# Performance work log

Hardware: AMD Instinct MI355X
Metric: run time of the kernel (lower is better)

Reference implementation:

```python
import jax, jax.numpy as jnp
import numpy as np

NBIT = 8
NSPLIT = 255.0  # 2**NBIT - 1


def _quantized_matmul(x, w_clean, eps):
    # Faithful port of quantization(): bit-slice x into NBIT binary planes, run a
    # noisy linear per plane with weight w + randn*|w|*0.1, and sum. The 8
    # sequential fc() calls are fused into one einsum over the bit axis.
    # x: (..., in); w_clean: (out, in); eps: (NBIT, out, in) standard normal.
    mn = jnp.min(x)
    mx = jnp.max(x)
    q = ((x - mn) / (mx - mn) * NSPLIT).astype(jnp.uint8).astype(jnp.int32)  # truncating cast as in torch
    quant_base = 2 ** jnp.arange(NBIT, dtype=jnp.int32)
    binary = ((q[..., None] & quant_base) != 0).astype(x.dtype)              # (..., in, NBIT)
    scaled = binary * (2.0 ** jnp.arange(NBIT)).astype(x.dtype)              # plane i scaled by 2**i
    w_noisy = w_clean[None] + eps * jnp.abs(w_clean)[None] * 0.1             # (NBIT, out, in)
    z = jnp.einsum('...ib,boi->...o', scaled, w_noisy)
    return z, mn, mx, w_noisy[-1]  # fc.weight after loop == last noisy weight


def _forward(node_embedding, edge_embedding, nbr_mask, cond1, cond2, eps1, eps2, bn_gamma, bn_beta):
    B, At, Nbr, Fe = edge_embedding.shape
    Fn = node_embedding.shape[-1]
    c1 = jnp.concatenate(
        [jnp.broadcast_to(node_embedding[:, :, None, :], (B, At, Nbr, Fn)), edge_embedding],
        axis=3)                                                              # (B, At, Nbr, Fn+Fe)
    # quantization + re_quantization through fc (re-quant uses last noisy fc.weight)
    z1, mn1, mx1, w_last = _quantized_matmul(c1, cond1[0], eps1)
    bias1 = jnp.sum(mn1 * w_last, axis=1)                                    # (H1,)
    h = jax.nn.relu(z1 / NSPLIT * (mx1 - mn1) + bias1)                       # (B, At, Nbr, H1)
    # quantization + re_quantization through fc_2 (re-quant uses conductance[1][-1])
    z2, mn2, mx2, _ = _quantized_matmul(h, cond2[0], eps2)
    bias2 = jnp.sum(mn2 * cond2[-1], axis=1)                                 # (2*Fn,)
    c2 = z2 / NSPLIT * (mx2 - mn2) + bias2                                   # (B, At, Nbr, 2*Fn)
    nbr_gate, nbr_extract = jnp.split(c2, 2, axis=3)
    nbr_sumed = jax.nn.sigmoid(nbr_gate) * jnp.tanh(nbr_extract) * nbr_mask[..., None]
    nbr_sumed = jnp.sum(nbr_sumed, axis=2)                                   # (B, At, Fn)
    # BatchNorm1d in training mode: batch statistics over flattened (B*At)
    flat = nbr_sumed.reshape(-1, Fn)
    mean = jnp.mean(flat, axis=0)
    var = jnp.var(flat, axis=0)  # biased variance, as torch BN uses for normalization
    bn = ((flat - mean) / jnp.sqrt(var + 1e-5) * bn_gamma + bn_beta).reshape(B, At, Fn)
    return jax.nn.relu(node_embedding + bn)


def setup_inputs() -> dict:
    key = jax.random.key(0)
    ks = jax.random.split(key, 7)
    B, At, Nbr, Fn, Fe = 16, 96, 12, 64, 64
    H1, H2 = 4 * (Fn + Fe), 2 * Fn
    return {
        'node_embedding': jax.random.normal(ks[0], (B, At, Fn), jnp.float32),
        'edge_embedding': jax.random.normal(ks[1], (B, At, Nbr, Fe), jnp.float32),
        'nbr_mask': (jax.random.uniform(ks[2], (B, At, Nbr)) > 0.5).astype(jnp.float32),
        'cond1': jax.random.normal(ks[3], (2, H1, Fn + Fe), jnp.float32) * 0.05,
        'cond2': jax.random.normal(ks[4], (2, H2, H1), jnp.float32) * 0.05,
        'eps1': jax.random.normal(ks[5], (NBIT, H1, Fn + Fe), jnp.float32),
        'eps2': jax.random.normal(ks[6], (NBIT, H2, H1), jnp.float32),
        'bn_gamma': jnp.ones((Fn,), jnp.float32),
        'bn_beta': jnp.zeros((Fn,), jnp.float32),
    }


def reference(node_embedding, edge_embedding, nbr_mask, cond1, cond2, eps1, eps2, bn_gamma, bn_beta):
    return _forward(node_embedding, edge_embedding, nbr_mask, cond1, cond2, eps1, eps2, bn_gamma, bn_beta)
```

## Files before the change

kernel.cpp:

```cpp
#include <hip/hip_runtime.h>
#include <stdint.h>

#define B_    16
#define AT_   96
#define NBR_  12
#define FN_   64
#define FE_   64
#define M1    (B_*AT_*NBR_)
#define R_    (B_*AT_)
#define K1Q   128
#define N1    512
#define K2Q   512
#define N2    128
#define SPLIT2 4

typedef _Float16 f16x8 __attribute__((ext_vector_type(8)));
typedef float    f32x4 __attribute__((ext_vector_type(4)));
typedef __attribute__((address_space(1))) const void gconst_void;
typedef __attribute__((address_space(3))) void lds_void;

#define OFF_SCAL  0u
#define OFF_B1R   256u
#define OFF_B2R   (OFF_B1R + 2048u)
#define OFF_Q1    4096u
#define OFF_W1E   (OFF_Q1  + (size_t)M1*K1Q)
#define OFF_W2E   (OFF_W1E + (size_t)N1*K1Q*8*2)
#define OFF_Q2    (OFF_W2E + (size_t)N2*K2Q*8*2)
#define OFF_H     (OFF_Q2  + (size_t)M1*K2Q)
#define OFF_ZP    OFF_H
#define OFF_NS    (OFF_H   + (size_t)M1*N1*4)

__device__ __forceinline__ unsigned int enc_f(float f) {
    unsigned int u = __float_as_uint(f);
    return (u & 0x80000000u) ? ~u : (u | 0x80000000u);
}
__device__ __forceinline__ float dec_f(unsigned int u) {
    return __uint_as_float((u & 0x80000000u) ? (u & 0x7FFFFFFFu) : ~u);
}

__global__ void k_init(unsigned int* scal, float* b1raw, float* b2raw) {
    int t = threadIdx.x;
    if (t == 0) { scal[0] = 0xFFFFFFFFu; scal[1] = 0u; scal[2] = 0xFFFFFFFFu; scal[3] = 0u; }
    if (t < N1) b1raw[t] = 0.f;
    if (t < N2) b2raw[t] = 0.f;
}

__global__ __launch_bounds__(256) void k_minmax_c1(const float* __restrict__ node,
                                                   const float* __restrict__ edge,
                                                   unsigned int* __restrict__ scal) {
    const int nn = B_*AT_*FN_;
    const int ntot = nn + M1*FE_;
    float mn = 3.0e38f, mx = -3.0e38f;
    for (int idx = blockIdx.x*blockDim.x + threadIdx.x; idx < ntot; idx += gridDim.x*blockDim.x) {
        float x = (idx < nn) ? node[idx] : edge[idx - nn];
        mn = fminf(mn, x); mx = fmaxf(mx, x);
    }
    __shared__ float smn[256], smx[256];
    smn[threadIdx.x] = mn; smx[threadIdx.x] = mx; __syncthreads();
    for (int s = 128; s > 0; s >>= 1) {
        if (threadIdx.x < s) {
            smn[threadIdx.x] = fminf(smn[threadIdx.x], smn[threadIdx.x+s]);
            smx[threadIdx.x] = fmaxf(smx[threadIdx.x], smx[threadIdx.x+s]);
        }
        __syncthreads();
    }
    if (threadIdx.x == 0) { atomicMin(&scal[0], enc_f(smn[0])); atomicMax(&scal[1], enc_f(smx[0])); }
}

template<int KQ, int N, int SBASE, bool USE_SECOND>
__global__ __launch_bounds__(256) void k_prep_w16(const float* __restrict__ w_clean,
                                                  const float* __restrict__ eps,
                                                  const unsigned int* __restrict__ scal,
                                                  float* __restrict__ braw,
                                                  _Float16* __restrict__ We) {
    int idx = blockIdx.x*blockDim.x + threadIdx.x;
    if (idx >= N*KQ) return;
    int o = idx / KQ;
    float mn = dec_f(scal[SBASE]), mx = dec_f(scal[SBASE+1]);
    float s = (mx - mn) * (1.0f/255.0f);
    float w = w_clean[idx];
    float aw = fabsf(w) * 0.1f;
    union { _Float16 h[8]; uint4 u; } pk;
    float p = s;
    float v7 = 0.f;
    #pragma unroll
    for (int b = 0; b < 8; b++) {
        float e = eps[(size_t)b*N*KQ + idx];
        float v = w + e*aw;
        if (b == 7) v7 = v;
        pk.h[b] = (_Float16)(v * p);
        p *= 2.0f;
    }
    *(uint4*)&We[(size_t)idx*8] = pk.u;
    float bv = USE_SECOND ? w_clean[(size_t)N*KQ + idx] : v7;
    #pragma unroll
    for (int off = 32; off > 0; off >>= 1) bv += __shfl_down(bv, off);
    if ((threadIdx.x & 63) == 0) atomicAdd(&braw[o], bv);
}

__global__ __launch_bounds__(256) void k_quant_c1(const float* __restrict__ node,
                                                  const float* __restrict__ edge,
                                                  const unsigned int* __restrict__ scal,
                                                  unsigned int* __restrict__ qt) {
    __shared__ unsigned int T[128*33];
    const int mblk = blockIdx.x, t = threadIdx.x;
    const float mn = dec_f(scal[0]), rng = dec_f(scal[1]) - mn;
    #pragma unroll
    for (int r = 0; r < 16; ++r) {
        int p = r*256 + t;
        int row = p >> 5, c4 = p & 31, j = c4*4;
        int m = mblk*128 + row;
        float4 x = (j < 64) ? *(const float4*)&node[(m/NBR_)*FN_ + j]
                            : *(const float4*)&edge[(size_t)m*FE_ + (j-64)];
        unsigned int b0 = (unsigned char)(int)((x.x - mn) / rng * 255.0f);
        unsigned int b1 = (unsigned char)(int)((x.y - mn) / rng * 255.0f);
        unsigned int b2 = (unsigned char)(int)((x.z - mn) / rng * 255.0f);
        unsigned int b3 = (unsigned char)(int)((x.w - mn) / rng * 255.0f);
        T[row*33 + c4] = b0 | (b1 << 8) | (b2 << 16) | (b3 << 24);
    }
    __syncthreads();
    #pragma unroll
    for (int r = 0; r < 16; ++r) {
        int o = r*256 + t;
        qt[(size_t)mblk*4096 + o] = T[(t>>1)*33 + r*2 + (t&1)];
    }
}

__global__ __launch_bounds__(256) void k_quant_h(const float* __restrict__ h,
                                                 const unsigned int* __restrict__ scal,
                                                 unsigned int* __restrict__ qt) {
    __shared__ unsigned int T[128*33];
    const int mblk = blockIdx.x, jc = blockIdx.y, t = threadIdx.x;
    const float mn = dec_f(scal[2]), rng = dec_f(scal[3]) - mn;
    #pragma unroll
    for (int r = 0; r < 16; ++r) {
        int p = r*256 + t;
        int row = p >> 5, c4 = p & 31;
        float4 x = *(const float4*)&h[(size_t)(mblk*128 + row)*512 + jc*128 + c4*4];
        unsigned int b0 = (unsigned char)(int)((x.x - mn) / rng * 255.0f);
        unsigned int b1 = (unsigned char)(int)((x.y - mn) / rng * 255.0f);
        unsigned int b2 = (unsigned char)(int)((x.z - mn) / rng * 255.0f);
        unsigned int b3 = (unsigned char)(int)((x.w - mn) / rng * 255.0f);
        T[row*33 + c4] = b0 | (b1 << 8) | (b2 << 16) | (b3 << 24);
    }
    __syncthreads();
    #pragma unroll
    for (int r = 0; r < 16; ++r) {
        int o = r*256 + t;
        qt[(size_t)mblk*16384 + (size_t)jc*4096 + o] = T[(t>>1)*33 + r*2 + (t&1)];
    }
}

__device__ __forceinline__ f16x8 expand_byte(unsigned int byte) {
    unsigned int r2 = byte | (byte << 15);
    union { unsigned int u[4]; f16x8 h; } t;
    t.u[0] = ( r2       & 0x00010001u) * 0x3C00u;
    t.u[1] = ((r2 >> 2) & 0x00010001u) * 0x3C00u;
    t.u[2] = ((r2 >> 4) & 0x00010001u) * 0x3C00u;
    t.u[3] = ((r2 >> 6) & 0x00010001u) * 0x3C00u;
    return t.h;
}

template<int KQ, int N, int SPLITK, bool EPI1>
__global__ __launch_bounds__(256, 4) void kg(const unsigned char* __restrict__ q,
                                             const _Float16* __restrict__ W,
                                             const float* __restrict__ braw,
                                             void* __restrict__ outv,
                                             unsigned int* __restrict__ scal) {
    constexpr int KP  = KQ * 8;
    constexpr int KPS = KP / SPLITK;
    constexpr int NIT = KPS / 128;
    __shared__ _Float16 Bs[16384];
    __shared__ __align__(16) unsigned char As[16384];

    const int tid  = threadIdx.x;
    const int lane = tid & 63;
    const int w    = tid >> 6;
    const int wm   = (w & 1) * 64;
    const int kg   = w >> 1;
    const int l15  = lane & 15;
    const int lq   = lane >> 4;
    const int sh8  = lq * 8;
    const int m0   = blockIdx.x * 128;
    const int o0   = blockIdx.y * 64;
    const int kbase = blockIdx.z * KPS;

    f32x4 acc[4][4] = {};

    unsigned int bo[4];
    #pragma unroll
    for (int iss = 0; iss < 4; ++iss) {
        int s = iss*256 + tid, skg = s >> 9, sg = s & 511, n = sg >> 3;
        int csrc = (sg & 7) ^ (n & 7);
        bo[iss] = (unsigned int)((o0 + n)*KP + kbase + skg*512 + csrc*8);
    }
    const int bdl = (tid & ~63) * 8;

    const unsigned char* aq = q + (size_t)blockIdx.x*((size_t)KQ*128) + (size_t)blockIdx.z*16384;
    #pragma unroll
    for (int r = 0; r < 4; ++r)
        __builtin_amdgcn_global_load_lds((gconst_void*)(aq + r*4096 + tid*16),
            (lds_void*)(As + r*4096 + (tid & ~63)*16), 16, 0, 0);

    auto stageB = [&](int IT, int BUF) {
        #pragma unroll
        for (int iss = 0; iss < 4; ++iss)
            __builtin_amdgcn_global_load_lds((gconst_void*)(W + bo[iss] + IT*64),
                (lds_void*)(Bs + BUF*8192 + iss*2048 + bdl), 16, 0, 0);
    };

    auto compute = [&](int cur, int it) {
        const _Float16* Bc = Bs + cur*8192 + kg*4096;
        const unsigned char* Ac = As + kg*8192 + it*1024;
        uint2 qd[4];
        #pragma unroll
        for (int mf = 0; mf < 4; ++mf)
            qd[mf] = *(const uint2*)&Ac[(wm + mf*16 + l15)*8];
        #pragma unroll
        for (int kf = 0; kf < 2; ++kf) {
            f16x8 bf[4];
            #pragma unroll
            for (int nf = 0; nf < 4; ++nf) {
                const int nl = nf*16 + l15;
                const int ch = kf*4 + lq;
                bf[nf] = *(const f16x8*)&Bc[nl*64 + ((ch ^ (nl & 7)) << 3)];
            }
            __builtin_amdgcn_s_setprio(1);
            #pragma unroll
            for (int mf = 0; mf < 4; ++mf) {
                unsigned int byte = ((kf ? qd[mf].y : qd[mf].x) >> sh8) & 0xFFu;
                f16x8 a = expand_byte(byte);
                #pragma unroll
                for (int nf = 0; nf < 4; ++nf)
                    acc[mf][nf] = __builtin_amdgcn_mfma_f32_16x16x32_f16(a, bf[nf], acc[mf][nf], 0, 0, 0);
            }
            __builtin_amdgcn_s_setprio(0);
        }
    };

    stageB(0, 0);
    #pragma unroll 1
    for (int it = 0; it < NIT-1; ++it) {
        const int cur = it & 1;
        stageB(it+1, cur ^ 1);
        asm volatile("s_waitcnt vmcnt(4)" ::: "memory");
        asm volatile("s_barrier" ::: "memory");
        compute(cur, it);
        asm volatile("s_waitcnt lgkmcnt(0)" ::: "memory");
        asm volatile("s_barrier" ::: "memory");
    }
    asm volatile("s_waitcnt vmcnt(0)" ::: "memory");
    asm volatile("s_barrier" ::: "memory");
    compute((NIT-1) & 1, NIT-1);

    float* red = (float*)Bs;
    #pragma unroll
    for (int nf = 0; nf < 4; ++nf) {
        __syncthreads();
        if (kg == 1) {
            #pragma unroll
            for (int mf = 0; mf < 4; ++mf)
                *(f32x4*)&red[(w & 1)*1024 + mf*256 + lane*4] = acc[mf][nf];
        }
        __syncthreads();
        if (kg == 0) {
            #pragma unroll
            for (int mf = 0; mf < 4; ++mf)
                acc[mf][nf] += *(const f32x4*)&red[(w & 1)*1024 + mf*256 + lane*4];
        }
    }

    if (EPI1) {
        float tmn = 3.0e38f, tmx = -3.0e38f;
        if (kg == 0) {
            float* out = (float*)outv;
            const float mn1 = dec_f(scal[0]);
            float bv[4];
            #pragma unroll
            for (int nf = 0; nf < 4; ++nf) bv[nf] = mn1 * braw[o0 + nf*16 + l15];
            #pragma unroll
            for (int mf = 0; mf < 4; ++mf) {
                const int mr = m0 + wm + mf*16 + lq*4;
                #pragma unroll
                for (int nf = 0; nf < 4; ++nf) {
                    const int oc = o0 + nf*16 + l15;
                    #pragma unroll
                    for (int r = 0; r < 4; ++r) {
                        float v = acc[mf][nf][r] + bv[nf];
                        v = fmaxf(v, 0.0f);
                        tmn = fminf(tmn, v); tmx = fmaxf(tmx, v);
                        out[(size_t)(mr + r)*N + oc] = v;
                    }
                }
            }
        }
        __syncthreads();
        red[tid] = tmn; red[256 + tid] = tmx;
        __syncthreads();
        for (int s = 128; s > 0; s >>= 1) {
            if (tid < s) {
                red[tid]       = fminf(red[tid],       red[tid + s]);
                red[256 + tid] = fmaxf(red[256 + tid], red[256 + tid + s]);
            }
            __syncthreads();
        }
        if (tid == 0) { atomicMin(&scal[2], enc_f(red[0])); atomicMax(&scal[3], enc_f(red[256])); }
    } else {
        if (kg == 0) {
            _Float16* op = (_Float16*)outv + (size_t)blockIdx.z * ((size_t)M1 * N);
            #pragma unroll
            for (int mf = 0; mf < 4; ++mf) {
                const int mr = m0 + wm + mf*16 + lq*4;
                #pragma unroll
                for (int nf = 0; nf < 4; ++nf) {
                    const int oc = o0 + nf*16 + l15;
                    #pragma unroll
                    for (int r = 0; r < 4; ++r)
                        op[(size_t)(mr + r)*N + oc] = (_Float16)acc[mf][nf][r];
                }
            }
        }
    }
}

__global__ __launch_bounds__(256) void k_nbr(const _Float16* __restrict__ zp,
                                             const float* __restrict__ b2raw,
                                             const unsigned int* __restrict__ scal,
                                             const float* __restrict__ mask,
                                             float* __restrict__ ns) {
    const size_t SP = (size_t)M1 * N2;
    int tid = threadIdx.x;
    int r = blockIdx.x*4 + (tid >> 6);
    int f = tid & 63;
    const float mn2 = dec_f(scal[2]);
    float bg = mn2 * b2raw[f], be = mn2 * b2raw[64 + f];
    float s = 0.f;
    #pragma unroll
    for (int n = 0; n < NBR_; n++) {
        int m = r*NBR_ + n;
        size_t base = (size_t)m * N2;
        float g = bg, e = be;
        #pragma unroll
        for (int z = 0; z < SPLIT2; z++) {
            g += (float)zp[z*SP + base + f];
            e += (float)zp[z*SP + base + 64 + f];
        }
        float sig = 1.0f / (1.0f + expf(-g));
        s += sig * tanhf(e) * mask[m];
    }
    ns[r*64 + f] = s;
}

__global__ __launch_bounds__(256) void k_bn(const float* __restrict__ ns,
                                            const float* __restrict__ node,
                                            const float* __restrict__ gamma,
                                            const float* __restrict__ beta,
                                            float* __restrict__ out) {
    int f = blockIdx.x;
    int tid = threadIdx.x;
    float x[6];
    float s = 0.f, ss = 0.f;
    #pragma unroll
    for (int k = 0; k < 6; k++) {
        int r = tid + k*256;
        x[k] = ns[r*64 + f];
        s += x[k]; ss += x[k]*x[k];
    }
    __shared__ float rs[256], rss[256];
    rs[tid] = s; rss[tid] = ss; __syncthreads();
    for (int st = 128; st > 0; st >>= 1) {
        if (tid < st) { rs[tid] += rs[tid+st]; rss[tid] += rss[tid+st]; }
        __syncthreads();
    }
    float mean = rs[0] / 1536.0f;
    float var  = rss[0] / 1536.0f - mean*mean;
    float denom = sqrtf(var + 1e-5f);
    float g = gamma[f], bt = beta[f];
    #pragma unroll
    for (int k = 0; k < 6; k++) {
        int r = tid + k*256;
        float v = node[r*64 + f] + ((x[k] - mean) / denom * g + bt);
        out[r*64 + f] = fmaxf(v, 0.f);
    }
}

extern "C" void kernel_launch(void* const* d_in, const int* in_sizes, int n_in,
                              void* d_out, int out_size, void* d_ws, size_t ws_size,
                              hipStream_t stream) {
    const float* node  = (const float*)d_in[0];
    const float* edge  = (const float*)d_in[1];
    const float* mask  = (const float*)d_in[2];
    const float* cond1 = (const float*)d_in[3];
    const float* cond2 = (const float*)d_in[4];
    const float* eps1  = (const float*)d_in[5];
    const float* eps2  = (const float*)d_in[6];
    const float* gamma = (const float*)d_in[7];
    const float* beta  = (const float*)d_in[8];
    float* out = (float*)d_out;
    char* ws = (char*)d_ws;

    unsigned int*  scal = (unsigned int*)(ws + OFF_SCAL);
    float* b1raw = (float*)(ws + OFF_B1R);
    float* b2raw = (float*)(ws + OFF_B2R);
    unsigned char* q1 = (unsigned char*)(ws + OFF_Q1);
    _Float16* W1e = (_Float16*)(ws + OFF_W1E);
    _Float16* W2e = (_Float16*)(ws + OFF_W2E);
    unsigned char* q2 = (unsigned char*)(ws + OFF_Q2);
    float*    h  = (float*)(ws + OFF_H);
    _Float16* zp = (_Float16*)(ws + OFF_ZP);
    float*    ns = (float*)(ws + OFF_NS);

    k_init<<<1, 1024, 0, stream>>>(scal, b1raw, b2raw);
    k_minmax_c1<<<512, 256, 0, stream>>>(node, edge, scal);
    k_prep_w16<K1Q, N1, 0, false><<<(N1*K1Q + 255)/256, 256, 0, stream>>>(cond1, eps1, scal, b1raw, W1e);
    k_quant_c1<<<M1/128, 256, 0, stream>>>(node, edge, scal, (unsigned int*)q1);
    kg<K1Q, N1, 1, true><<<dim3(M1/128, N1/64, 1), 256, 0, stream>>>(q1, W1e, b1raw, h, scal);
    k_prep_w16<K2Q, N2, 2, true><<<(N2*K2Q + 255)/256, 256, 0, stream>>>(cond2, eps2, scal, b2raw, W2e);
    k_quant_h<<<dim3(M1/128, 4), 256, 0, stream>>>(h, scal, (unsigned int*)q2);
    kg<K2Q, N2, SPLIT2, false><<<dim3(M1/128, N2/64, SPLIT2), 256, 0, stream>>>(q2, W2e, b2raw, zp, scal);
    k_nbr<<<R_/4, 256, 0, stream>>>(zp, b2raw, scal, mask, ns);
    k_bn<<<64, 256, 0, stream>>>(ns, node, gamma, beta, out);
}
```

Baseline: 218.5 us.

## Replace LDS-staged block GEMM with single-wave direct-global-load GEMM

The bit-plane GEMM moves from 256-thread blocks, which stage A and B tiles through LDS with double buffering, intra-block split-K and an LDS reduction, to single-wave 64-thread blocks. Each wave now loads its A bytes and B fragments straight from global memory into registers and computes a 64x64 tile over the full K slice. The LDS barriers, the cross-wave reduction and the tree min/max are dropped, and the min/max uses a wave shuffle reduction instead. The cost is less data reuse through LDS, so more global and L2 traffic from uncoalesced per-lane fragment loads. It also gives up the explicit prefetch pipelining and launches more, smaller blocks.

Result: slower. 280.0 us (+28.2%).

```diff
diff --git a/kernel.cpp b/kernel.cpp
--- a/kernel.cpp
+++ b/kernel.cpp
@@ -16,8 +16,6 @@
 
 typedef _Float16 f16x8 __attribute__((ext_vector_type(8)));
 typedef float    f32x4 __attribute__((ext_vector_type(4)));
-typedef __attribute__((address_space(1))) const void gconst_void;
-typedef __attribute__((address_space(3))) void lds_void;
 
 #define OFF_SCAL  0u
 #define OFF_B1R   256u
@@ -162,70 +160,44 @@
 }
 
 template<int KQ, int N, int SPLITK, bool EPI1>
-__global__ __launch_bounds__(256, 4) void kg(const unsigned char* __restrict__ q,
+__global__ __launch_bounds__(64, 4) void kgw(const unsigned char* __restrict__ q,
                                              const _Float16* __restrict__ W,
                                              const float* __restrict__ braw,
                                              void* __restrict__ outv,
                                              unsigned int* __restrict__ scal) {
     constexpr int KP  = KQ * 8;
     constexpr int KPS = KP / SPLITK;
-    constexpr int NIT = KPS / 128;
-    __shared__ _Float16 Bs[16384];
-    __shared__ __align__(16) unsigned char As[16384];
-
-    const int tid  = threadIdx.x;
-    const int lane = tid & 63;
-    const int w    = tid >> 6;
-    const int wm   = (w & 1) * 64;
-    const int kg   = w >> 1;
-    const int l15  = lane & 15;
-    const int lq   = lane >> 4;
-    const int sh8  = lq * 8;
-    const int m0   = blockIdx.x * 128;
-    const int o0   = blockIdx.y * 64;
-    const int kbase = blockIdx.z * KPS;
+    constexpr int NJG = KPS / 64;
+
+    const int lane = threadIdx.x;
+    const int l15 = lane & 15;
+    const int lq  = lane >> 4;
+    const int sh8 = lq * 8;
+    const int mt  = blockIdx.x;
+    const int o0  = blockIdx.y * 64;
+    const int z   = blockIdx.z;
 
     f32x4 acc[4][4] = {};
 
-    unsigned int bo[4];
-    #pragma unroll
-    for (int iss = 0; iss < 4; ++iss) {
-        int s = iss*256 + tid, skg = s >> 9, sg = s & 511, n = sg >> 3;
-        int csrc = (sg & 7) ^ (n & 7);
-        bo[iss] = (unsigned int)((o0 + n)*KP + kbase + skg*512 + csrc*8);
-    }
-    const int bdl = (tid & ~63) * 8;
-
-    const unsigned char* aq = q + (size_t)blockIdx.x*((size_t)KQ*128) + (size_t)blockIdx.z*16384;
-    #pragma unroll
-    for (int r = 0; r < 4; ++r)
-        __builtin_amdgcn_global_load_lds((gconst_void*)(aq + r*4096 + tid*16),
-            (lds_void*)(As + r*4096 + (tid & ~63)*16), 16, 0, 0);
-
-    auto stageB = [&](int IT, int BUF) {
-        #pragma unroll
-        for (int iss = 0; iss < 4; ++iss)
-            __builtin_amdgcn_global_load_lds((gconst_void*)(W + bo[iss] + IT*64),
-                (lds_void*)(Bs + BUF*8192 + iss*2048 + bdl), 16, 0, 0);
-    };
-
-    auto compute = [&](int cur, int it) {
-        const _Float16* Bc = Bs + cur*8192 + kg*4096;
-        const unsigned char* Ac = As + kg*8192 + it*1024;
+    const unsigned char* aq = q + (size_t)(mt >> 1)*((size_t)KQ*128)
+                                + (size_t)z*16384 + ((mt & 1)*64 + l15)*8;
+    const _Float16* wn[4];
+    #pragma unroll
+    for (int nf = 0; nf < 4; ++nf)
+        wn[nf] = W + (size_t)(o0 + nf*16 + l15)*KP + (size_t)z*KPS + lq*8;
+
+    #pragma unroll 2
+    for (int jg = 0; jg < NJG; ++jg) {
         uint2 qd[4];
         #pragma unroll
         for (int mf = 0; mf < 4; ++mf)
-            qd[mf] = *(const uint2*)&Ac[(wm + mf*16 + l15)*8];
+            qd[mf] = *(const uint2*)(aq + jg*1024 + mf*128);
         #pragma unroll
         for (int kf = 0; kf < 2; ++kf) {
             f16x8 bf[4];
             #pragma unroll
-            for (int nf = 0; nf < 4; ++nf) {
-                const int nl = nf*16 + l15;
-                const int ch = kf*4 + lq;
-                bf[nf] = *(const f16x8*)&Bc[nl*64 + ((ch ^ (nl & 7)) << 3)];
-            }
-            __builtin_amdgcn_s_setprio(1);
+            for (int nf = 0; nf < 4; ++nf)
+                bf[nf] = *(const f16x8*)(wn[nf] + jg*64 + kf*32);
             #pragma unroll
             for (int mf = 0; mf < 4; ++mf) {
                 unsigned int byte = ((kf ? qd[mf].y : qd[mf].x) >> sh8) & 0xFFu;
@@ -234,90 +206,48 @@
                 for (int nf = 0; nf < 4; ++nf)
                     acc[mf][nf] = __builtin_amdgcn_mfma_f32_16x16x32_f16(a, bf[nf], acc[mf][nf], 0, 0, 0);
             }
-            __builtin_amdgcn_s_setprio(0);
-        }
-    };
-
-    stageB(0, 0);
-    #pragma unroll 1
-    for (int it = 0; it < NIT-1; ++it) {
-        const int cur = it & 1;
-        stageB(it+1, cur ^ 1);
-        asm volatile("s_waitcnt vmcnt(4)" ::: "memory");
-        asm volatile("s_barrier" ::: "memory");
-        compute(cur, it);
-        asm volatile("s_waitcnt lgkmcnt(0)" ::: "memory");
-        asm volatile("s_barrier" ::: "memory");
-    }
-    asm volatile("s_waitcnt vmcnt(0)" ::: "memory");
-    asm volatile("s_barrier" ::: "memory");
-    compute((NIT-1) & 1, NIT-1);
-
-    float* red = (float*)Bs;
-    #pragma unroll
-    for (int nf = 0; nf < 4; ++nf) {
-        __syncthreads();
-        if (kg == 1) {
+        }
+    }
+
+    if (EPI1) {
+        float* out = (float*)outv;
+        const float mn1 = dec_f(scal[0]);
+        float bv[4];
+        #pragma unroll
+        for (int nf = 0; nf < 4; ++nf) bv[nf] = mn1 * braw[o0 + nf*16 + l15];
+        float tmn = 3.0e38f, tmx = -3.0e38f;
+        #pragma unroll
+        for (int mf = 0; mf < 4; ++mf) {
+            const int mr = mt*64 + mf*16 + lq*4;
             #pragma unroll
-            for (int mf = 0; mf < 4; ++mf)
-                *(f32x4*)&red[(w & 1)*1024 + mf*256 + lane*4] = acc[mf][nf];
-        }
-        __syncthreads();
-        if (kg == 0) {
-            #pragma unroll
-            for (int mf = 0; mf < 4; ++mf)
-                acc[mf][nf] += *(const f32x4*)&red[(w & 1)*1024 + mf*256 + lane*4];
-        }
-    }
-
-    if (EPI1) {
-        float tmn = 3.0e38f, tmx = -3.0e38f;
-        if (kg == 0) {
-            float* out = (float*)outv;
-            const float mn1 = dec_f(scal[0]);
-            float bv[4];
-            #pragma unroll
-            for (int nf = 0; nf < 4; ++nf) bv[nf] = mn1 * braw[o0 + nf*16 + l15];
-            #pragma unroll
-            for (int mf = 0; mf < 4; ++mf) {
-                const int mr = m0 + wm + mf*16 + lq*4;
+            for (int nf = 0; nf < 4; ++nf) {
+                const int oc = o0 + nf*16 + l15;
                 #pragma unroll
-                for (int nf = 0; nf < 4; ++nf) {
-                    const int oc = o0 + nf*16 + l15;
-                    #pragma unroll
-                    for (int r = 0; r < 4; ++r) {
-                        float v = acc[mf][nf][r] + bv[nf];
-                        v = fmaxf(v, 0.0f);
-                        tmn = fminf(tmn, v); tmx = fmaxf(tmx, v);
-                        out[(size_t)(mr + r)*N + oc] = v;
-                    }
+                for (int r = 0; r < 4; ++r) {
+                    float v = acc[mf][nf][r] + bv[nf];
+                    v = fmaxf(v, 0.0f);
+                    tmn = fminf(tmn, v); tmx = fmaxf(tmx, v);
+                    out[(size_t)(mr + r)*N + oc] = v;
                 }
             }
         }
-        __syncthreads();
-        red[tid] = tmn; red[256 + tid] = tmx;
-        __syncthreads();
-        for (int s = 128; s > 0; s >>= 1) {
-            if (tid < s) {
-                red[tid]       = fminf(red[tid],       red[tid + s]);
-                red[256 + tid] = fmaxf(red[256 + tid], red[256 + tid + s]);
-            }
-            __syncthreads();
-        }
-        if (tid == 0) { atomicMin(&scal[2], enc_f(red[0])); atomicMax(&scal[3], enc_f(red[256])); }
+        #pragma unroll
+        for (int off = 32; off > 0; off >>= 1) {
+            tmn = fminf(tmn, __shfl_xor(tmn, off));
+            tmx = fmaxf(tmx, __shfl_xor(tmx, off));
+        }
+        if (lane == 0) { atomicMin(&scal[2], enc_f(tmn)); atomicMax(&scal[3], enc_f(tmx)); }
     } else {
-        if (kg == 0) {
-            _Float16* op = (_Float16*)outv + (size_t)blockIdx.z * ((size_t)M1 * N);
+        _Float16* op = (_Float16*)outv + (size_t)z * ((size_t)M1 * N);
+        #pragma unroll
+        for (int mf = 0; mf < 4; ++mf) {
+            const int mr = mt*64 + mf*16 + lq*4;
             #pragma unroll
-            for (int mf = 0; mf < 4; ++mf) {
-                const int mr = m0 + wm + mf*16 + lq*4;
+            for (int nf = 0; nf < 4; ++nf) {
+                const int oc = o0 + nf*16 + l15;
                 #pragma unroll
-                for (int nf = 0; nf < 4; ++nf) {
-                    const int oc = o0 + nf*16 + l15;
-                    #pragma unroll
-                    for (int r = 0; r < 4; ++r)
-                        op[(size_t)(mr + r)*N + oc] = (_Float16)acc[mf][nf][r];
-                }
+                for (int r = 0; r < 4; ++r)
+                    op[(size_t)(mr + r)*N + oc] = (_Float16)acc[mf][nf][r];
             }
         }
     }
@@ -414,10 +344,10 @@
     k_minmax_c1<<<512, 256, 0, stream>>>(node, edge, scal);
     k_prep_w16<K1Q, N1, 0, false><<<(N1*K1Q + 255)/256, 256, 0, stream>>>(cond1, eps1, scal, b1raw, W1e);
     k_quant_c1<<<M1/128, 256, 0, stream>>>(node, edge, scal, (unsigned int*)q1);
-    kg<K1Q, N1, 1, true><<<dim3(M1/128, N1/64, 1), 256, 0, stream>>>(q1, W1e, b1raw, h, scal);
+    kgw<K1Q, N1, 1, true><<<dim3(M1/64, N1/64, 1), 64, 0, stream>>>(q1, W1e, b1raw, h, scal);
     k_prep_w16<K2Q, N2, 2, true><<<(N2*K2Q + 255)/256, 256, 0, stream>>>(cond2, eps2, scal, b2raw, W2e);
     k_quant_h<<<dim3(M1/128, 4), 256, 0, stream>>>(h, scal, (unsigned int*)q2);
-    kg<K2Q, N2, SPLIT2, false><<<dim3(M1/128, N2/64, SPLIT2), 256, 0, stream>>>(q2, W2e, b2raw, zp, scal);
+    kgw<K2Q, N2, SPLIT2, false><<<dim3(M1/64, N2/64, SPLIT2), 64, 0, stream>>>(q2, W2e, b2raw, zp, scal);
     k_nbr<<<R_/4, 256, 0, stream>>>(zp, b2raw, scal, mask, ns);
     k_bn<<<64, 256, 0, stream>>>(ns, node, gamma, beta, out);
 }
```

## Split GEMM warps over N, triple-buffer B tiles, add XCD-aware block swizzle

Applied to the files above, without the earlier changes.

The GEMM kernel no longer splits K across warp pairs, which required an LDS reduction at the end. The four warps now split the N dimension, each computing a 64x32 tile. B staging moves to a 3-deep ring of 64-wide K chunks, so compute overlaps with two outstanding prefetches. The 3D grid becomes a 1D grid whose block index is remapped to group neighbouring tiles on the same XCD for L2 reuse. In exchange there are twice as many K iterations, each with more barriers, and every wave now does per-wave epilogue stores.

After: 212.5 us. 2.7% less time.

```diff
diff --git a/kernel.cpp b/kernel.cpp
--- a/kernel.cpp
+++ b/kernel.cpp
@@ -162,66 +162,80 @@
 }
 
 template<int KQ, int N, int SPLITK, bool EPI1>
-__global__ __launch_bounds__(256, 4) void kg(const unsigned char* __restrict__ q,
-                                             const _Float16* __restrict__ W,
-                                             const float* __restrict__ braw,
-                                             void* __restrict__ outv,
-                                             unsigned int* __restrict__ scal) {
+__global__ __launch_bounds__(256, 4) void kgp(const unsigned char* __restrict__ q,
+                                              const _Float16* __restrict__ W,
+                                              const float* __restrict__ braw,
+                                              void* __restrict__ outv,
+                                              unsigned int* __restrict__ scal) {
     constexpr int KP  = KQ * 8;
     constexpr int KPS = KP / SPLITK;
-    constexpr int NIT = KPS / 128;
-    __shared__ _Float16 Bs[16384];
+    constexpr int NIT = KPS / 64;
+    constexpr int NT  = N / 64;
+    constexpr int NMB = M1 / 128;
+    constexpr int CPX = NMB * NT * SPLITK / 8;
+    __shared__ _Float16 Bs[3*4096];
     __shared__ __align__(16) unsigned char As[16384];
 
     const int tid  = threadIdx.x;
     const int lane = tid & 63;
     const int w    = tid >> 6;
     const int wm   = (w & 1) * 64;
-    const int kg   = w >> 1;
+    const int wn   = (w >> 1) * 32;
     const int l15  = lane & 15;
     const int lq   = lane >> 4;
     const int sh8  = lq * 8;
-    const int m0   = blockIdx.x * 128;
-    const int o0   = blockIdx.y * 64;
-    const int kbase = blockIdx.z * KPS;
-
-    f32x4 acc[4][4] = {};
-
-    unsigned int bo[4];
-    #pragma unroll
-    for (int iss = 0; iss < 4; ++iss) {
-        int s = iss*256 + tid, skg = s >> 9, sg = s & 511, n = sg >> 3;
-        int csrc = (sg & 7) ^ (n & 7);
-        bo[iss] = (unsigned int)((o0 + n)*KP + kbase + skg*512 + csrc*8);
+
+    const int lin = blockIdx.x;
+    const int swz = (lin & 7) * CPX + (lin >> 3);
+    const int x   = swz % NMB;
+    const int c   = swz / NMB;
+    const int y   = c % NT;
+    const int z   = c / NT;
+    const int m0  = x * 128;
+    const int o0  = y * 64;
+    const int kbase = z * KPS;
+
+    f32x4 acc[4][2] = {};
+
+    unsigned int boff[2];
+    #pragma unroll
+    for (int iss = 0; iss < 2; ++iss) {
+        int s = iss*256 + tid, n = s >> 3, cc = s & 7;
+        int csrc = cc ^ (n & 7);
+        boff[iss] = (unsigned int)((o0 + n)*KP + kbase + csrc*8);
     }
     const int bdl = (tid & ~63) * 8;
 
-    const unsigned char* aq = q + (size_t)blockIdx.x*((size_t)KQ*128) + (size_t)blockIdx.z*16384;
+    auto stageB = [&](int it, int cb) {
+        #pragma unroll
+        for (int iss = 0; iss < 2; ++iss)
+            __builtin_amdgcn_global_load_lds((gconst_void*)(W + boff[iss] + it*64),
+                (lds_void*)(Bs + cb*4096 + iss*2048 + bdl), 16, 0, 0);
+    };
+
+    const unsigned char* aq = q + (size_t)x*((size_t)KQ*128) + (size_t)z*16384;
     #pragma unroll
     for (int r = 0; r < 4; ++r)
         __builtin_amdgcn_global_load_lds((gconst_void*)(aq + r*4096 + tid*16),
             (lds_void*)(As + r*4096 + (tid & ~63)*16), 16, 0, 0);
-
-    auto stageB = [&](int IT, int BUF) {
-        #pragma unroll
-        for (int iss = 0; iss < 4; ++iss)
-            __builtin_amdgcn_global_load_lds((gconst_void*)(W + bo[iss] + IT*64),
-                (lds_void*)(Bs + BUF*8192 + iss*2048 + bdl), 16, 0, 0);
-    };
-
-    auto compute = [&](int cur, int it) {
-        const _Float16* Bc = Bs + cur*8192 + kg*4096;
-        const unsigned char* Ac = As + kg*8192 + it*1024;
+    stageB(0, 0);
+    stageB(1, 1);
+    stageB(2, 2);
+    asm volatile("s_waitcnt vmcnt(4)" ::: "memory");
+    asm volatile("s_barrier" ::: "memory");
+
+    auto compute = [&](int cb, int it) {
+        const _Float16* Bc = Bs + cb*4096;
         uint2 qd[4];
         #pragma unroll
         for (int mf = 0; mf < 4; ++mf)
-            qd[mf] = *(const uint2*)&Ac[(wm + mf*16 + l15)*8];
+            qd[mf] = *(const uint2*)&As[it*1024 + (wm + mf*16 + l15)*8];
         #pragma unroll
         for (int kf = 0; kf < 2; ++kf) {
-            f16x8 bf[4];
+            f16x8 bf[2];
             #pragma unroll
-            for (int nf = 0; nf < 4; ++nf) {
-                const int nl = nf*16 + l15;
+            for (int nf = 0; nf < 2; ++nf) {
+                const int nl = wn + nf*16 + l15;
                 const int ch = kf*4 + lq;
                 bf[nf] = *(const f16x8*)&Bc[nl*64 + ((ch ^ (nl & 7)) << 3)];
             }
@@ -231,70 +245,62 @@
                 unsigned int byte = ((kf ? qd[mf].y : qd[mf].x) >> sh8) & 0xFFu;
                 f16x8 a = expand_byte(byte);
                 #pragma unroll
-                for (int nf = 0; nf < 4; ++nf)
+                for (int nf = 0; nf < 2; ++nf)
                     acc[mf][nf] = __builtin_amdgcn_mfma_f32_16x16x32_f16(a, bf[nf], acc[mf][nf], 0, 0, 0);
             }
             __builtin_amdgcn_s_setprio(0);
         }
     };
 
-    stageB(0, 0);
+    int cb = 0;
     #pragma unroll 1
-    for (int it = 0; it < NIT-1; ++it) {
-        const int cur = it & 1;
-        stageB(it+1, cur ^ 1);
+    for (int it = 0; it < NIT-3; ++it) {
+        compute(cb, it);
+        asm volatile("s_waitcnt lgkmcnt(0)" ::: "memory");
+        asm volatile("s_barrier" ::: "memory");
+        stageB(it+3, cb);
         asm volatile("s_waitcnt vmcnt(4)" ::: "memory");
         asm volatile("s_barrier" ::: "memory");
-        compute(cur, it);
-        asm volatile("s_waitcnt lgkmcnt(0)" ::: "memory");
-        asm volatile("s_barrier" ::: "memory");
-    }
+        cb = (cb == 2) ? 0 : cb + 1;
+    }
+    compute(cb, NIT-3);
+    asm volatile("s_waitcnt lgkmcnt(0)" ::: "memory");
+    asm volatile("s_barrier" ::: "memory");
+    asm volatile("s_waitcnt vmcnt(2)" ::: "memory");
+    asm volatile("s_barrier" ::: "memory");
+    cb = (cb == 2) ? 0 : cb + 1;
+    compute(cb, NIT-2);
+    asm volatile("s_waitcnt lgkmcnt(0)" ::: "memory");
+    asm volatile("s_barrier" ::: "memory");
     asm volatile("s_waitcnt vmcnt(0)" ::: "memory");
     asm volatile("s_barrier" ::: "memory");
-    compute((NIT-1) & 1, NIT-1);
-
-    float* red = (float*)Bs;
-    #pragma unroll
-    for (int nf = 0; nf < 4; ++nf) {
-        __syncthreads();
-        if (kg == 1) {
+    cb = (cb == 2) ? 0 : cb + 1;
+    compute(cb, NIT-1);
+
+    if (EPI1) {
+        float* out = (float*)outv;
+        const float mn1 = dec_f(scal[0]);
+        float bv[2];
+        #pragma unroll
+        for (int nf = 0; nf < 2; ++nf) bv[nf] = mn1 * braw[o0 + wn + nf*16 + l15];
+        float tmn = 3.0e38f, tmx = -3.0e38f;
+        #pragma unroll
+        for (int mf = 0; mf < 4; ++mf) {
+            const int mr = m0 + wm + mf*16 + lq*4;
             #pragma unroll
-            for (int mf = 0; mf < 4; ++mf)
-                *(f32x4*)&red[(w & 1)*1024 + mf*256 + lane*4] = acc[mf][nf];
-        }
-        __syncthreads();
-        if (kg == 0) {
-            #pragma unroll
-            for (int mf = 0; mf < 4; ++mf)
-                acc[mf][nf] += *(const f32x4*)&red[(w & 1)*1024 + mf*256 + lane*4];
-        }
-    }
-
-    if (EPI1) {
-        float tmn = 3.0e38f, tmx = -3.0e38f;
-        if (kg == 0) {
-            float* out = (float*)outv;
-            const float mn1 = dec_f(scal[0]);
-            float bv[4];
-            #pragma unroll
-            for (int nf = 0; nf < 4; ++nf) bv[nf] = mn1 * braw[o0 + nf*16 + l15];
-            #pragma unroll
-            for (int mf = 0; mf < 4; ++mf) {
-                const int mr = m0 + wm + mf*16 + lq*4;
+            for (int nf = 0; nf < 2; ++nf) {
+                const int oc = o0 + wn + nf*16 + l15;
                 #pragma unroll
-                for (int nf = 0; nf < 4; ++nf) {
-                    const int oc = o0 + nf*16 + l15;
-                    #pragma unroll
-                    for (int r = 0; r < 4; ++r) {
-                        float v = acc[mf][nf][r] + bv[nf];
-                        v = fmaxf(v, 0.0f);
-                        tmn = fminf(tmn, v); tmx = fmaxf(tmx, v);
-                        out[(size_t)(mr + r)*N + oc] = v;
-                    }
+                for (int r = 0; r < 4; ++r) {
+                    float v = acc[mf][nf][r] + bv[nf];
+                    v = fmaxf(v, 0.0f);
+                    tmn = fminf(tmn, v); tmx = fmaxf(tmx, v);
+                    out[(size_t)(mr + r)*N + oc] = v;
                 }
             }
         }
         __syncthreads();
+        float* red = (float*)Bs;
         red[tid] = tmn; red[256 + tid] = tmx;
         __syncthreads();
         for (int s = 128; s > 0; s >>= 1) {
@@ -306,18 +312,16 @@
         }
         if (tid == 0) { atomicMin(&scal[2], enc_f(red[0])); atomicMax(&scal[3], enc_f(red[256])); }
     } else {
-        if (kg == 0) {
-            _Float16* op = (_Float16*)outv + (size_t)blockIdx.z * ((size_t)M1 * N);
+        _Float16* op = (_Float16*)outv + (size_t)z * ((size_t)M1 * N);
+        #pragma unroll
+        for (int mf = 0; mf < 4; ++mf) {
+            const int mr = m0 + wm + mf*16 + lq*4;
             #pragma unroll
-            for (int mf = 0; mf < 4; ++mf) {
-                const int mr = m0 + wm + mf*16 + lq*4;
+            for (int nf = 0; nf < 2; ++nf) {
+                const int oc = o0 + wn + nf*16 + l15;
                 #pragma unroll
-                for (int nf = 0; nf < 4; ++nf) {
-                    const int oc = o0 + nf*16 + l15;
-                    #pragma unroll
-                    for (int r = 0; r < 4; ++r)
-                        op[(size_t)(mr + r)*N + oc] = (_Float16)acc[mf][nf][r];
-                }
+                for (int r = 0; r < 4; ++r)
+                    op[(size_t)(mr + r)*N + oc] = (_Float16)acc[mf][nf][r];
             }
         }
     }
@@ -414,10 +418,10 @@
     k_minmax_c1<<<512, 256, 0, stream>>>(node, edge, scal);
     k_prep_w16<K1Q, N1, 0, false><<<(N1*K1Q + 255)/256, 256, 0, stream>>>(cond1, eps1, scal, b1raw, W1e);
     k_quant_c1<<<M1/128, 256, 0, stream>>>(node, edge, scal, (unsigned int*)q1);
-    kg<K1Q, N1, 1, true><<<dim3(M1/128, N1/64, 1), 256, 0, stream>>>(q1, W1e, b1raw, h, scal);
+    kgp<K1Q, N1, 1, true><<<(M1/128)*(N1/64), 256, 0, stream>>>(q1, W1e, b1raw, h, scal);
     k_prep_w16<K2Q, N2, 2, true><<<(N2*K2Q + 255)/256, 256, 0, stream>>>(cond2, eps2, scal, b2raw, W2e);
     k_quant_h<<<dim3(M1/128, 4), 256, 0, stream>>>(h, scal, (unsigned int*)q2);
-    kg<K2Q, N2, SPLIT2, false><<<dim3(M1/128, N2/64, SPLIT2), 256, 0, stream>>>(q2, W2e, b2raw, zp, scal);
+    kgp<K2Q, N2, SPLIT2, false><<<(M1/128)*(N2/64)*SPLIT2, 256, 0, stream>>>(q2, W2e, b2raw, zp, scal);
     k_nbr<<<R_/4, 256, 0, stream>>>(zp, b2raw, scal, mask, ns);
     k_bn<<<64, 256, 0, stream>>>(ns, node, gamma, beta, out);
 }
```
